# Kernel optimization log

Hardware: AMD Instinct MI355X
Metric: run time of the kernel (lower is better)

The kernel has to match this reference:

```python
import jax, jax.numpy as jnp
import numpy as np

NORM_EPS = 1e-5
HEAD_DIM = 32
SR_RATIO = 2
N_RATIO = SR_RATIO ** 2  # avg-pool kernel/stride over sequence


def setup_inputs() -> dict:
    key = jax.random.key(0)
    ks = jax.random.split(key, 12)
    B, N, C = 4, 3136, 384
    s = 0.02
    inp = {
        "x": jax.random.normal(ks[0], (B, N, C), dtype=jnp.float32),
        "Wq": jax.random.normal(ks[1], (C, C), dtype=jnp.float32) * s,
        "bq": jnp.zeros((C,), jnp.float32),
        "Wk": jax.random.normal(ks[2], (C, C), dtype=jnp.float32) * s,
        "bk": jnp.zeros((C,), jnp.float32),
        "Wv": jax.random.normal(ks[3], (C, C), dtype=jnp.float32) * s,
        "bv": jnp.zeros((C,), jnp.float32),
        "Wp": jax.random.normal(ks[4], (C, C), dtype=jnp.float32) * s,
        "bp": jnp.zeros((C,), jnp.float32),
        "bn_gamma": jnp.ones((C,), jnp.float32),
        "bn_beta": jnp.zeros((C,), jnp.float32),
        "bn_mean": jax.random.normal(ks[5], (C,), dtype=jnp.float32) * 0.1,
        "bn_var": jax.random.uniform(ks[6], (C,), dtype=jnp.float32, minval=0.5, maxval=1.5),
    }
    return inp


def reference(x, Wq, bq, Wk, bk, Wv, bv, Wp, bp, bn_gamma, bn_beta, bn_mean, bn_var):
    B, N, C = x.shape
    H = C // HEAD_DIM
    d = HEAD_DIM
    scale = d ** -0.5

    # q projection -> [B, H, N, d]
    q = (x @ Wq.T + bq).reshape(B, N, H, d)

    # sequence reduction: AvgPool1d(kernel=stride=N_RATIO) over tokens
    Nk = N // N_RATIO
    x_ = x.reshape(B, Nk, N_RATIO, C).mean(axis=2)  # [B, Nk, C]
    # BatchNorm1d over channel dim (inference / running-stats form)
    x_ = (x_ - bn_mean) * jax.lax.rsqrt(bn_var + NORM_EPS) * bn_gamma + bn_beta

    k = (x_ @ Wk.T + bk).reshape(B, Nk, H, d)
    v = (x_ @ Wv.T + bv).reshape(B, Nk, H, d)

    attn = jnp.einsum("bnhd,bmhd->bhnm", q, k) * scale  # [B, H, N, Nk]
    attn = jax.nn.softmax(attn, axis=-1)
    out = jnp.einsum("bhnm,bmhd->bnhd", attn, v).reshape(B, N, C)
    return out @ Wp.T + bp
```

## Files before the change

### kernel.cpp

```cpp
#include <hip/hip_runtime.h>


typedef __bf16 bf16x8 __attribute__((ext_vector_type(8)));
typedef unsigned short u16x8 __attribute__((ext_vector_type(8)));
typedef float f32x4 __attribute__((ext_vector_type(4)));

#define NTOK 3136
#define NKV 784
#define CCH 384
#define KPAD 832
#define SC2 0.25503472078024693f

#define WAIT_BAR(N) asm volatile("s_waitcnt vmcnt(" #N ")\n\ts_barrier" ::: "memory")

__device__ __forceinline__ unsigned short f2b(float f) {
  union { float f; unsigned u; } v; v.f = f;
  unsigned r = v.u + 0x7fffu + ((v.u >> 16) & 1u);
  return (unsigned short)(r >> 16);
}

__device__ __forceinline__ bf16x8 ldsb8(const unsigned short* p) {
  u16x8 v = *(const u16x8*)p;
  return __builtin_bit_cast(bf16x8, v);
}

__device__ __forceinline__ void gload16(const void* g, void* lds) {
  auto* g1 = reinterpret_cast<const __attribute__((address_space(1))) unsigned int*>(
      reinterpret_cast<uintptr_t>(g));
  auto* l3 = reinterpret_cast<__attribute__((address_space(3))) unsigned int*>(
      reinterpret_cast<uintptr_t>(lds));
  __builtin_amdgcn_global_load_lds(g1, l3, 16, 0, 0);
}

__global__ __launch_bounds__(256) void prep_kernel(
    const float* __restrict__ x, const float* __restrict__ gam,
    const float* __restrict__ bet, const float* __restrict__ mea,
    const float* __restrict__ var,
    const float* __restrict__ Wq, const float* __restrict__ Wk,
    const float* __restrict__ Wv, const float* __restrict__ Wp,
    unsigned short* __restrict__ xb, unsigned short* __restrict__ xpb,
    unsigned short* __restrict__ wq, unsigned short* __restrict__ wk,
    unsigned short* __restrict__ wv, unsigned short* __restrict__ wp,
    unsigned short* __restrict__ vt) {
  int bid = blockIdx.x;
  if (bid < 1176) {
    int i = bid * 256 + threadIdx.x;
    int c4 = i % 96;
    int row = i / 96;
    int b = row / NKV, nk = row - b * NKV;
    const float4* x4 = (const float4*)x;
    size_t base = ((size_t)(b * NTOK + nk * 4)) * 96 + c4;
    float sx = 0.f, sy = 0.f, sz = 0.f, sw = 0.f;
#pragma unroll
    for (int r = 0; r < 4; ++r) {
      float4 v = x4[base + (size_t)r * 96];
      ushort4 cv; cv.x = f2b(v.x); cv.y = f2b(v.y); cv.z = f2b(v.z); cv.w = f2b(v.w);
      ((ushort4*)xb)[base + (size_t)r * 96] = cv;
      sx += v.x; sy += v.y; sz += v.z; sw += v.w;
    }
    float4 g4 = ((const float4*)gam)[c4];
    float4 b4 = ((const float4*)bet)[c4];
    float4 m4 = ((const float4*)mea)[c4];
    float4 v4 = ((const float4*)var)[c4];
    ushort4 r4;
    r4.x = f2b((sx * 0.25f - m4.x) * rsqrtf(v4.x + 1e-5f) * g4.x + b4.x);
    r4.y = f2b((sy * 0.25f - m4.y) * rsqrtf(v4.y + 1e-5f) * g4.y + b4.y);
    r4.z = f2b((sz * 0.25f - m4.z) * rsqrtf(v4.z + 1e-5f) * g4.z + b4.z);
    r4.w = f2b((sw * 0.25f - m4.w) * rsqrtf(v4.w + 1e-5f) * g4.w + b4.w);
    ((ushort4*)xpb)[i] = r4;
  } else if (bid < 1320) {
    int i = (bid - 1176) * 256 + threadIdx.x;
    float4 va = ((const float4*)Wq)[i];
    float4 vb = ((const float4*)Wk)[i];
    float4 vc = ((const float4*)Wv)[i];
    float4 vd = ((const float4*)Wp)[i];
    ushort4 ra; ra.x = f2b(va.x); ra.y = f2b(va.y); ra.z = f2b(va.z); ra.w = f2b(va.w);
    ushort4 rb; rb.x = f2b(vb.x); rb.y = f2b(vb.y); rb.z = f2b(vb.z); rb.w = f2b(vb.w);
    ushort4 rc; rc.x = f2b(vc.x); rc.y = f2b(vc.y); rc.z = f2b(vc.z); rc.w = f2b(vc.w);
    ushort4 rd; rd.x = f2b(vd.x); rd.y = f2b(vd.y); rd.z = f2b(vd.z); rd.w = f2b(vd.w);
    ((ushort4*)wq)[i] = ra; ((ushort4*)wk)[i] = rb;
    ((ushort4*)wv)[i] = rc; ((ushort4*)wp)[i] = rd;
  } else {
    int i = (bid - 1320) * 256 + threadIdx.x;
    int row = i >> 4, quad = i & 15;
    ushort4 z; z.x = 0; z.y = 0; z.z = 0; z.w = 0;
    *(ushort4*)&vt[(size_t)row * KPAD + 768 + quad * 4] = z;
  }
}

__device__ __forceinline__ void gemm_body(
    const unsigned short* __restrict__ A, const unsigned short* __restrict__ Bt,
    const float* __restrict__ bias, void* __restrict__ out,
    int row0, int col0, int epi, float oscale,
    unsigned short (*sA)[2048], unsigned short (*sB)[4096]) {
  const int t = threadIdx.x, w = t >> 6, l = t & 63;
  const int wr = w >> 1, wc = w & 1;

  f32x4 acc[2][4];
#pragma unroll
  for (int m = 0; m < 2; ++m)
#pragma unroll
    for (int n = 0; n < 4; ++n) acc[m][n] = (f32x4){0.f, 0.f, 0.f, 0.f};

  const unsigned short* Abase = A + (size_t)(row0 + l) * CCH + w * 8;
  const unsigned short* B0base = Bt + (size_t)(col0 + l) * CCH + w * 8;
  const unsigned short* B1base = Bt + (size_t)(col0 + 64 + l) * CCH + w * 8;

  auto STAGE = [&](int kk, int bsel) {
    gload16(Abase + kk * 32, (char*)sA[bsel] + w * 1024);
    gload16(B0base + kk * 32, (char*)sB[bsel] + w * 2048);
    gload16(B1base + kk * 32, (char*)sB[bsel] + w * 2048 + 1024);
  };

  STAGE(0, 0);
  STAGE(1, 1);
  WAIT_BAR(3);

#pragma unroll
  for (int kk = 0; kk < 12; ++kk) {
    const int cur = kk % 3;
    const int stg = (kk + 2) % 3;
    if (kk + 2 < 12) STAGE(kk + 2, stg);
    bf16x8 af[2], bfv[4];
#pragma unroll
    for (int m = 0; m < 2; ++m)
      af[m] = ldsb8(&sA[cur][(l >> 4) * 512 + (wr * 32 + m * 16 + (l & 15)) * 8]);
#pragma unroll
    for (int n = 0; n < 4; ++n)
      bfv[n] = ldsb8(&sB[cur][(l >> 4) * 1024 + (wc * 64 + n * 16 + (l & 15)) * 8]);
#pragma unroll
    for (int m = 0; m < 2; ++m)
#pragma unroll
      for (int n = 0; n < 4; ++n)
        acc[m][n] = __builtin_amdgcn_mfma_f32_16x16x32_bf16(af[m], bfv[n], acc[m][n], 0, 0, 0);
    if (kk + 1 < 12) {
      if (kk + 2 < 12) WAIT_BAR(3); else WAIT_BAR(0);
    }
  }

#pragma unroll
  for (int m = 0; m < 2; ++m) {
#pragma unroll
    for (int r = 0; r < 4; ++r) {
      int row = row0 + wr * 32 + m * 16 + (l >> 4) * 4 + r;
#pragma unroll
      for (int n = 0; n < 4; ++n) {
        int col = col0 + wc * 64 + n * 16 + (l & 15);
        float v = (acc[m][n][r] + bias[col]) * oscale;
        if (epi == 0) {
          ((unsigned short*)out)[(size_t)row * CCH + col] =
              __builtin_bit_cast(unsigned short, (__bf16)v);
        } else if (epi == 2) {
          ((float*)out)[(size_t)row * CCH + col] = v;
        } else {
          int b_ = row / NKV, j = row - b_ * NKV;
          int h_ = col >> 5, d = col & 31;
          int loc = j & 63;
          int kap = (j & ~63) + ((loc & 16) << 1) + ((loc & 12) << 1) +
                    ((loc & 32) >> 3) + (loc & 3);
          ((unsigned short*)out)[((size_t)((b_ * 12 + h_) * 32 + d)) * KPAD + kap] =
              __builtin_bit_cast(unsigned short, (__bf16)v);
        }
      }
    }
  }
}

__global__ __launch_bounds__(256) void qkv_kernel(
    const unsigned short* __restrict__ xb, const unsigned short* __restrict__ xpb,
    const unsigned short* __restrict__ wq, const unsigned short* __restrict__ wk,
    const unsigned short* __restrict__ wv,
    const float* __restrict__ bq, const float* __restrict__ bk,
    const float* __restrict__ bv,
    unsigned short* __restrict__ q_b, unsigned short* __restrict__ k_b,
    unsigned short* __restrict__ vt_b) {
  __shared__ unsigned short sA[3][2048];
  __shared__ unsigned short sB[3][4096];
  int bx = blockIdx.x;
  const unsigned short *Ap, *Wp_;
  const float* bp_;
  void* op;
  int epi, row0;
  float osc;
  if (bx < 196)      { Ap = xb;  Wp_ = wq; bp_ = bq; op = q_b;  epi = 0; row0 = bx * 64;         osc = SC2; }
  else if (bx < 245) { Ap = xpb; Wp_ = wk; bp_ = bk; op = k_b;  epi = 0; row0 = (bx - 196) * 64; osc = 1.f; }
  else               { Ap = xpb; Wp_ = wv; bp_ = bv; op = vt_b; epi = 1; row0 = (bx - 245) * 64; osc = 1.f; }
  gemm_body(Ap, Wp_, bp_, op, row0, blockIdx.y * 128, epi, osc, sA, sB);
}

__global__ __launch_bounds__(256) void outproj_kernel(
    const unsigned short* __restrict__ ob, const unsigned short* __restrict__ wp,
    const float* __restrict__ bp_, float* __restrict__ out) {
  __shared__ unsigned short sA[3][2048];
  __shared__ unsigned short sB[3][4096];
  gemm_body(ob, wp, bp_, (void*)out, blockIdx.x * 64, blockIdx.y * 128, 2, 1.f, sA, sB);
}

__global__ __launch_bounds__(256) void attn_kernel(
    const unsigned short* __restrict__ qb, const unsigned short* __restrict__ kb,
    const unsigned short* __restrict__ vtb, unsigned short* __restrict__ ob) {
  __shared__ unsigned short sQ[2048];
  __shared__ unsigned short sK[3][2048];
  __shared__ unsigned short sV[3][2048];

  const int bx = blockIdx.x;
  const int qt = bx % 49;
  const int h = (bx / 49) % 12;
  const int b = bx / 588;
  const int t = threadIdx.x, w = t >> 6, l = t & 63;
  const int q0 = qt * 64;
  const int hi = l >> 4, c = l & 15;

  const unsigned short* vbase = vtb + ((size_t)((b * 12 + h) * 32 + (l & 31))) * KPAD
                                + (2 * w + (l >> 5)) * 8;

  auto stageK = [&](int ttile, int bsel) {
    int j = ttile * 64 + l; if (j > NKV - 1) j = NKV - 1;
    gload16(kb + ((size_t)(b * NKV + j)) * CCH + h * 32 + w * 8,
            (char*)sK[bsel] + w * 1024);
  };
  auto stageV = [&](int ttile, int bsel) {
    gload16(vbase + ttile * 64, (char*)sV[bsel] + w * 1024);
  };

  gload16(qb + ((size_t)(b * NTOK + q0 + l)) * CCH + h * 32 + w * 8,
          (char*)sQ + w * 1024);
  stageK(0, 0); stageV(0, 0);
  stageK(1, 1); stageV(1, 1);
  WAIT_BAR(2);

  const bf16x8 aq = ldsb8(&sQ[hi * 512 + (w * 16 + c) * 8]);
  bf16x8 ones;
#pragma unroll
  for (int i = 0; i < 8; ++i) ones[i] = (__bf16)1.0f;
  const f32x4 fz = (f32x4){0.f, 0.f, 0.f, 0.f};

  f32x4 acc0 = fz, acc1 = fz, accl = fz;

#pragma unroll
  for (int tt = 0; tt < 13; ++tt) {
    const int cur = tt % 3;
    const int stg = (tt + 2) % 3;
    if (tt + 2 < 13) { stageK(tt + 2, stg); stageV(tt + 2, stg); }

    f32x4 s[4];
#pragma unroll
    for (int n = 0; n < 4; ++n) {
      bf16x8 kf = ldsb8(&sK[cur][hi * 512 + (n * 16 + c) * 8]);
      s[n] = __builtin_amdgcn_mfma_f32_16x16x32_bf16(kf, aq, fz, 0, 0, 0);
    }

    float p[4][4];
#pragma unroll
    for (int n = 0; n < 4; ++n)
#pragma unroll
      for (int r = 0; r < 4; ++r) {
        float e;
        asm("v_exp_f32 %0, %1" : "=v"(e) : "v"(s[n][r]));
        p[n][r] = e;
      }
    if (tt == 12) {
#pragma unroll
      for (int n = 1; n < 4; ++n)
#pragma unroll
        for (int r = 0; r < 4; ++r) p[n][r] = 0.f;
    }

    bf16x8 pa0, pa1;
#pragma unroll
    for (int rr = 0; rr < 4; ++rr) {
      pa0[rr] = (__bf16)p[0][rr];
      pa0[4 + rr] = (__bf16)p[2][rr];
      pa1[rr] = (__bf16)p[1][rr];
      pa1[4 + rr] = (__bf16)p[3][rr];
    }

#pragma unroll
    for (int kkk = 0; kkk < 2; ++kkk) {
      bf16x8 pa = kkk ? pa1 : pa0;
      bf16x8 v0 = ldsb8(&sV[cur][(kkk * 4 + hi) * 256 + c * 8]);
      bf16x8 v1 = ldsb8(&sV[cur][(kkk * 4 + hi) * 256 + (16 + c) * 8]);
      acc0 = __builtin_amdgcn_mfma_f32_16x16x32_bf16(pa, v0, acc0, 0, 0, 0);
      acc1 = __builtin_amdgcn_mfma_f32_16x16x32_bf16(pa, v1, acc1, 0, 0, 0);
      accl = __builtin_amdgcn_mfma_f32_16x16x32_bf16(pa, ones, accl, 0, 0, 0);
    }

    if (tt + 1 < 13) {
      if (tt + 2 < 13) WAIT_BAR(2); else WAIT_BAR(0);
    }
  }

#pragma unroll
  for (int r = 0; r < 4; ++r) {
    int row = q0 + w * 16 + hi * 4 + r;
    float inv = 1.f / accl[r];
    size_t base = ((size_t)(b * NTOK + row)) * CCH + h * 32;
    ob[base + c] = __builtin_bit_cast(unsigned short, (__bf16)(acc0[r] * inv));
    ob[base + 16 + c] = __builtin_bit_cast(unsigned short, (__bf16)(acc1[r] * inv));
  }
}


extern "C" void kernel_launch(void* const* d_in, const int* in_sizes, int n_in,
                              void* d_out, int out_size, void* d_ws, size_t ws_size,
                              hipStream_t stream) {
  const float* x   = (const float*)d_in[0];
  const float* Wq  = (const float*)d_in[1];
  const float* bq  = (const float*)d_in[2];
  const float* Wk  = (const float*)d_in[3];
  const float* bk  = (const float*)d_in[4];
  const float* Wv  = (const float*)d_in[5];
  const float* bv  = (const float*)d_in[6];
  const float* Wp  = (const float*)d_in[7];
  const float* bp  = (const float*)d_in[8];
  const float* gam = (const float*)d_in[9];
  const float* bet = (const float*)d_in[10];
  const float* mea = (const float*)d_in[11];
  const float* var = (const float*)d_in[12];

  unsigned short* wq_b = (unsigned short*)d_ws;
  unsigned short* wk_b = wq_b + 147456;
  unsigned short* wv_b = wk_b + 147456;
  unsigned short* wp_b = wv_b + 147456;
  unsigned short* xb   = wp_b + 147456;
  unsigned short* x_b  = xb + 12544 * 384;
  unsigned short* q_b  = x_b + 3136 * 384;
  unsigned short* k_b  = q_b + 12544 * 384;
  unsigned short* vt_b = k_b + 3136 * 384;
  unsigned short* o_b  = vt_b + 1536 * KPAD;

  prep_kernel<<<1416, 256, 0, stream>>>(x, gam, bet, mea, var, Wq, Wk, Wv, Wp,
                                        xb, x_b, wq_b, wk_b, wv_b, wp_b, vt_b);
  qkv_kernel<<<dim3(294, 3), 256, 0, stream>>>(xb, x_b, wq_b, wk_b, wv_b,
                                               bq, bk, bv, q_b, k_b, vt_b);
  attn_kernel<<<2352, 256, 0, stream>>>(q_b, k_b, vt_b, o_b);
  outproj_kernel<<<dim3(196, 3), 256, 0, stream>>>(o_b, wp_b, bp, (float*)d_out);
}
```

Before: 95.00 us.

## Double row tiles to 128 in Q/out-proj GEMMs and attention query tiles

Templates the GEMM body on the row-tile size, so the Q projection and the output projection use 128-row tiles while the K/V projections keep 64 rows. The attention kernel now handles 128 query rows per block with two Q fragments, so each staged K/V tile is reused for twice as many queries, with clamped loads and a guarded store for the partial last tile. The intent is to cut redundant global and LDS loads of weights and K/V and to lower block count overhead. In exchange the grids are smaller, which may hurt load balance and occupancy, and register and LDS use per block goes up.

```diff
diff --git a/kernel.cpp b/kernel.cpp
--- a/kernel.cpp
+++ b/kernel.cpp
@@ -88,64 +88,79 @@
   }
 }
 
+template <int MR>
 __device__ __forceinline__ void gemm_body(
     const unsigned short* __restrict__ A, const unsigned short* __restrict__ Bt,
     const float* __restrict__ bias, void* __restrict__ out,
     int row0, int col0, int epi, float oscale,
-    unsigned short (*sA)[2048], unsigned short (*sB)[4096]) {
+    unsigned short* sA, unsigned short* sB) {
+  constexpr int ABUF = MR * 32;
+  constexpr int MH = MR / 2;
+  constexpr int NM = MR / 32;
   const int t = threadIdx.x, w = t >> 6, l = t & 63;
   const int wr = w >> 1, wc = w & 1;
-
-  f32x4 acc[2][4];
-#pragma unroll
-  for (int m = 0; m < 2; ++m)
+  const int hi = l >> 4, c = l & 15;
+
+  f32x4 acc[NM][4];
+#pragma unroll
+  for (int m = 0; m < NM; ++m)
 #pragma unroll
     for (int n = 0; n < 4; ++n) acc[m][n] = (f32x4){0.f, 0.f, 0.f, 0.f};
 
   const unsigned short* Abase = A + (size_t)(row0 + l) * CCH + w * 8;
+  const unsigned short* Abase2 = A + (size_t)(row0 + 64 + l) * CCH + w * 8;
   const unsigned short* B0base = Bt + (size_t)(col0 + l) * CCH + w * 8;
   const unsigned short* B1base = Bt + (size_t)(col0 + 64 + l) * CCH + w * 8;
 
   auto STAGE = [&](int kk, int bsel) {
-    gload16(Abase + kk * 32, (char*)sA[bsel] + w * 1024);
-    gload16(B0base + kk * 32, (char*)sB[bsel] + w * 2048);
-    gload16(B1base + kk * 32, (char*)sB[bsel] + w * 2048 + 1024);
+    if constexpr (MR == 128) {
+      gload16(Abase + kk * 32, (char*)(sA + bsel * ABUF) + w * 2048);
+      gload16(Abase2 + kk * 32, (char*)(sA + bsel * ABUF) + w * 2048 + 1024);
+    } else {
+      gload16(Abase + kk * 32, (char*)(sA + bsel * ABUF) + w * 1024);
+    }
+    gload16(B0base + kk * 32, (char*)(sB + bsel * 4096) + w * 2048);
+    gload16(B1base + kk * 32, (char*)(sB + bsel * 4096) + w * 2048 + 1024);
   };
 
   STAGE(0, 0);
   STAGE(1, 1);
-  WAIT_BAR(3);
+  if constexpr (MR == 128) WAIT_BAR(4); else WAIT_BAR(3);
 
 #pragma unroll
   for (int kk = 0; kk < 12; ++kk) {
     const int cur = kk % 3;
     const int stg = (kk + 2) % 3;
     if (kk + 2 < 12) STAGE(kk + 2, stg);
-    bf16x8 af[2], bfv[4];
-#pragma unroll
-    for (int m = 0; m < 2; ++m)
-      af[m] = ldsb8(&sA[cur][(l >> 4) * 512 + (wr * 32 + m * 16 + (l & 15)) * 8]);
+    bf16x8 af[NM], bfv[4];
+#pragma unroll
+    for (int m = 0; m < NM; ++m)
+      af[m] = ldsb8(sA + cur * ABUF + hi * (MR * 8) + (wr * MH + m * 16 + c) * 8);
 #pragma unroll
     for (int n = 0; n < 4; ++n)
-      bfv[n] = ldsb8(&sB[cur][(l >> 4) * 1024 + (wc * 64 + n * 16 + (l & 15)) * 8]);
-#pragma unroll
-    for (int m = 0; m < 2; ++m)
+      bfv[n] = ldsb8(sB + cur * 4096 + hi * 1024 + (wc * 64 + n * 16 + c) * 8);
+#pragma unroll
+    for (int m = 0; m < NM; ++m)
 #pragma unroll
       for (int n = 0; n < 4; ++n)
         acc[m][n] = __builtin_amdgcn_mfma_f32_16x16x32_bf16(af[m], bfv[n], acc[m][n], 0, 0, 0);
     if (kk + 1 < 12) {
-      if (kk + 2 < 12) WAIT_BAR(3); else WAIT_BAR(0);
-    }
-  }
-
-#pragma unroll
-  for (int m = 0; m < 2; ++m) {
+      if (kk + 2 < 12) {
+        if constexpr (MR == 128) WAIT_BAR(4); else WAIT_BAR(3);
+      } else {
+        WAIT_BAR(0);
+      }
+    }
+  }
+
+#pragma unroll
+  for (int m = 0; m < NM; ++m) {
 #pragma unroll
     for (int r = 0; r < 4; ++r) {
-      int row = row0 + wr * 32 + m * 16 + (l >> 4) * 4 + r;
+      int row = row0 + wr * MH + m * 16 + hi * 4 + r;
 #pragma unroll
       for (int n = 0; n < 4; ++n) {
-        int col = col0 + wc * 64 + n * 16 + (l & 15);
+        int col = col0 + wc * 64 + n * 16 + c;
         float v = (acc[m][n][r] + bias[col]) * oscale;
         if (epi == 0) {
           ((unsigned short*)out)[(size_t)row * CCH + col] =
@@ -174,41 +189,40 @@
     const float* __restrict__ bv,
     unsigned short* __restrict__ q_b, unsigned short* __restrict__ k_b,
     unsigned short* __restrict__ vt_b) {
-  __shared__ unsigned short sA[3][2048];
-  __shared__ unsigned short sB[3][4096];
-  int bx = blockIdx.x;
-  const unsigned short *Ap, *Wp_;
-  const float* bp_;
-  void* op;
-  int epi, row0;
-  float osc;
-  if (bx < 196)      { Ap = xb;  Wp_ = wq; bp_ = bq; op = q_b;  epi = 0; row0 = bx * 64;         osc = SC2; }
-  else if (bx < 245) { Ap = xpb; Wp_ = wk; bp_ = bk; op = k_b;  epi = 0; row0 = (bx - 196) * 64; osc = 1.f; }
-  else               { Ap = xpb; Wp_ = wv; bp_ = bv; op = vt_b; epi = 1; row0 = (bx - 245) * 64; osc = 1.f; }
-  gemm_body(Ap, Wp_, bp_, op, row0, blockIdx.y * 128, epi, osc, sA, sB);
+  __shared__ unsigned short sA[3 * 4096];
+  __shared__ unsigned short sB[3 * 4096];
+  int bx = blockIdx.x, cy = blockIdx.y * 128;
+  if (bx < 98) {
+    gemm_body<128>(xb, wq, bq, (void*)q_b, bx * 128, cy, 0, SC2, sA, sB);
+  } else if (bx < 147) {
+    gemm_body<64>(xpb, wk, bk, (void*)k_b, (bx - 98) * 64, cy, 0, 1.f, sA, sB);
+  } else {
+    gemm_body<64>(xpb, wv, bv, (void*)vt_b, (bx - 147) * 64, cy, 1, 1.f, sA, sB);
+  }
 }
 
 __global__ __launch_bounds__(256) void outproj_kernel(
     const unsigned short* __restrict__ ob, const unsigned short* __restrict__ wp,
     const float* __restrict__ bp_, float* __restrict__ out) {
-  __shared__ unsigned short sA[3][2048];
-  __shared__ unsigned short sB[3][4096];
-  gemm_body(ob, wp, bp_, (void*)out, blockIdx.x * 64, blockIdx.y * 128, 2, 1.f, sA, sB);
+  __shared__ unsigned short sA[3 * 4096];
+  __shared__ unsigned short sB[3 * 4096];
+  gemm_body<128>(ob, wp, bp_, (void*)out, blockIdx.x * 128, blockIdx.y * 128, 2, 1.f,
+                 sA, sB);
 }
 
 __global__ __launch_bounds__(256) void attn_kernel(
     const unsigned short* __restrict__ qb, const unsigned short* __restrict__ kb,
     const unsigned short* __restrict__ vtb, unsigned short* __restrict__ ob) {
-  __shared__ unsigned short sQ[2048];
+  __shared__ unsigned short sQ[4096];
   __shared__ unsigned short sK[3][2048];
   __shared__ unsigned short sV[3][2048];
 
   const int bx = blockIdx.x;
-  const int qt = bx % 49;
-  const int h = (bx / 49) % 12;
-  const int b = bx / 588;
+  const int qt = bx % 25;
+  const int h = (bx / 25) % 12;
+  const int b = bx / 300;
   const int t = threadIdx.x, w = t >> 6, l = t & 63;
-  const int q0 = qt * 64;
+  const int q0 = qt * 128;
   const int hi = l >> 4, c = l & 15;
 
   const unsigned short* vbase = vtb + ((size_t)((b * 12 + h) * 32 + (l & 31))) * KPAD
@@ -223,19 +237,27 @@
     gload16(vbase + ttile * 64, (char*)sV[bsel] + w * 1024);
   };
 
-  gload16(qb + ((size_t)(b * NTOK + q0 + l)) * CCH + h * 32 + w * 8,
-          (char*)sQ + w * 1024);
+  {
+    int r0 = q0 + l;            if (r0 > NTOK - 1) r0 = NTOK - 1;
+    int r1 = q0 + 64 + l;       if (r1 > NTOK - 1) r1 = NTOK - 1;
+    gload16(qb + ((size_t)(b * NTOK + r0)) * CCH + h * 32 + w * 8,
+            (char*)sQ + w * 1024);
+    gload16(qb + ((size_t)(b * NTOK + r1)) * CCH + h * 32 + w * 8,
+            (char*)sQ + 4096 + w * 1024);
+  }
   stageK(0, 0); stageV(0, 0);
   stageK(1, 1); stageV(1, 1);
   WAIT_BAR(2);
 
-  const bf16x8 aq = ldsb8(&sQ[hi * 512 + (w * 16 + c) * 8]);
+  const bf16x8 aq0 = ldsb8(&sQ[hi * 512 + (w * 16 + c) * 8]);
+  const bf16x8 aq1 = ldsb8(&sQ[2048 + hi * 512 + (w * 16 + c) * 8]);
   bf16x8 ones;
 #pragma unroll
   for (int i = 0; i < 8; ++i) ones[i] = (__bf16)1.0f;
   const f32x4 fz = (f32x4){0.f, 0.f, 0.f, 0.f};
 
-  f32x4 acc0 = fz, acc1 = fz, accl = fz;
+  f32x4 a00 = fz, a01 = fz, al0 = fz;
+  f32x4 a10 = fz, a11 = fz, al1 = fz;
 
 #pragma unroll
   for (int tt = 0; tt < 13; ++tt) {
@@ -243,46 +265,70 @@
     const int stg = (tt + 2) % 3;
     if (tt + 2 < 13) { stageK(tt + 2, stg); stageV(tt + 2, stg); }
 
-    f32x4 s[4];
+    f32x4 s0[4], s1[4];
 #pragma unroll
     for (int n = 0; n < 4; ++n) {
       bf16x8 kf = ldsb8(&sK[cur][hi * 512 + (n * 16 + c) * 8]);
-      s[n] = __builtin_amdgcn_mfma_f32_16x16x32_bf16(kf, aq, fz, 0, 0, 0);
-    }
-
-    float p[4][4];
-#pragma unroll
-    for (int n = 0; n < 4; ++n)
-#pragma unroll
-      for (int r = 0; r < 4; ++r) {
-        float e;
-        asm("v_exp_f32 %0, %1" : "=v"(e) : "v"(s[n][r]));
-        p[n][r] = e;
+      s0[n] = __builtin_amdgcn_mfma_f32_16x16x32_bf16(kf, aq0, fz, 0, 0, 0);
+      s1[n] = __builtin_amdgcn_mfma_f32_16x16x32_bf16(kf, aq1, fz, 0, 0, 0);
+    }
+
+    bf16x8 pa00, pa01, pa10, pa11;
+    {
+      float p[4][4];
+#pragma unroll
+      for (int n = 0; n < 4; ++n)
+#pragma unroll
+        for (int r = 0; r < 4; ++r) {
+          float e;
+          asm("v_exp_f32 %0, %1" : "=v"(e) : "v"(s0[n][r]));
+          p[n][r] = e;
+        }
+      if (tt == 12)
+#pragma unroll
+        for (int n = 1; n < 4; ++n)
+#pragma unroll
+          for (int r = 0; r < 4; ++r) p[n][r] = 0.f;
+#pragma unroll
+      for (int rr = 0; rr < 4; ++rr) {
+        pa00[rr] = (__bf16)p[0][rr]; pa00[4 + rr] = (__bf16)p[2][rr];
+        pa01[rr] = (__bf16)p[1][rr]; pa01[4 + rr] = (__bf16)p[3][rr];
       }
-    if (tt == 12) {
-#pragma unroll
-      for (int n = 1; n < 4; ++n)
-#pragma unroll
-        for (int r = 0; r < 4; ++r) p[n][r] = 0.f;
-    }
-
-    bf16x8 pa0, pa1;
-#pragma unroll
-    for (int rr = 0; rr < 4; ++rr) {
-      pa0[rr] = (__bf16)p[0][rr];
-      pa0[4 + rr] = (__bf16)p[2][rr];
-      pa1[rr] = (__bf16)p[1][rr];
-      pa1[4 + rr] = (__bf16)p[3][rr];
+    }
+    {
+      float p[4][4];
+#pragma unroll
+      for (int n = 0; n < 4; ++n)
+#pragma unroll
+        for (int r = 0; r < 4; ++r) {
+          float e;
+          asm("v_exp_f32 %0, %1" : "=v"(e) : "v"(s1[n][r]));
+          p[n][r] = e;
+        }
+      if (tt == 12)
+#pragma unroll
+        for (int n = 1; n < 4; ++n)
+#pragma unroll
+          for (int r = 0; r < 4; ++r) p[n][r] = 0.f;
+#pragma unroll
+      for (int rr = 0; rr < 4; ++rr) {
+        pa10[rr] = (__bf16)p[0][rr]; pa10[4 + rr] = (__bf16)p[2][rr];
+        pa11[rr] = (__bf16)p[1][rr]; pa11[4 + rr] = (__bf16)p[3][rr];
+      }
     }
 
 #pragma unroll
     for (int kkk = 0; kkk < 2; ++kkk) {
-      bf16x8 pa = kkk ? pa1 : pa0;
+      bf16x8 pg0 = kkk ? pa01 : pa00;
+      bf16x8 pg1 = kkk ? pa11 : pa10;
       bf16x8 v0 = ldsb8(&sV[cur][(kkk * 4 + hi) * 256 + c * 8]);
       bf16x8 v1 = ldsb8(&sV[cur][(kkk * 4 + hi) * 256 + (16 + c) * 8]);
-      acc0 = __builtin_amdgcn_mfma_f32_16x16x32_bf16(pa, v0, acc0, 0, 0, 0);
-      acc1 = __builtin_amdgcn_mfma_f32_16x16x32_bf16(pa, v1, acc1, 0, 0, 0);
-      accl = __builtin_amdgcn_mfma_f32_16x16x32_bf16(pa, ones, accl, 0, 0, 0);
+      a00 = __builtin_amdgcn_mfma_f32_16x16x32_bf16(pg0, v0, a00, 0, 0, 0);
+      a10 = __builtin_amdgcn_mfma_f32_16x16x32_bf16(pg1, v0, a10, 0, 0, 0);
+      a01 = __builtin_amdgcn_mfma_f32_16x16x32_bf16(pg0, v1, a01, 0, 0, 0);
+      a11 = __builtin_amdgcn_mfma_f32_16x16x32_bf16(pg1, v1, a11, 0, 0, 0);
+      al0 = __builtin_amdgcn_mfma_f32_16x16x32_bf16(pg0, ones, al0, 0, 0, 0);
+      al1 = __builtin_amdgcn_mfma_f32_16x16x32_bf16(pg1, ones, al1, 0, 0, 0);
     }
 
     if (tt + 1 < 13) {
@@ -293,10 +339,20 @@
 #pragma unroll
   for (int r = 0; r < 4; ++r) {
     int row = q0 + w * 16 + hi * 4 + r;
-    float inv = 1.f / accl[r];
+    float inv = 1.f / al0[r];
     size_t base = ((size_t)(b * NTOK + row)) * CCH + h * 32;
-    ob[base + c] = __builtin_bit_cast(unsigned short, (__bf16)(acc0[r] * inv));
-    ob[base + 16 + c] = __builtin_bit_cast(unsigned short, (__bf16)(acc1[r] * inv));
+    ob[base + c] = __builtin_bit_cast(unsigned short, (__bf16)(a00[r] * inv));
+    ob[base + 16 + c] = __builtin_bit_cast(unsigned short, (__bf16)(a01[r] * inv));
+  }
+#pragma unroll
+  for (int r = 0; r < 4; ++r) {
+    int row = q0 + 64 + w * 16 + hi * 4 + r;
+    if (row < NTOK) {
+      float inv = 1.f / al1[r];
+      size_t base = ((size_t)(b * NTOK + row)) * CCH + h * 32;
+      ob[base + c] = __builtin_bit_cast(unsigned short, (__bf16)(a10[r] * inv));
+      ob[base + 16 + c] = __builtin_bit_cast(unsigned short, (__bf16)(a11[r] * inv));
+    }
   }
 }
 
@@ -331,8 +387,8 @@
 
   prep_kernel<<<1416, 256, 0, stream>>>(x, gam, bet, mea, var, Wq, Wk, Wv, Wp,
                                         xb, x_b, wq_b, wk_b, wv_b, wp_b, vt_b);
-  qkv_kernel<<<dim3(294, 3), 256, 0, stream>>>(xb, x_b, wq_b, wk_b, wv_b,
+  qkv_kernel<<<dim3(196, 3), 256, 0, stream>>>(xb, x_b, wq_b, wk_b, wv_b,
                                                bq, bk, bv, q_b, k_b, vt_b);
-  attn_kernel<<<2352, 256, 0, stream>>>(q_b, k_b, vt_b, o_b);
-  outproj_kernel<<<dim3(196, 3), 256, 0, stream>>>(o_b, wp_b, bp, (float*)d_out);
-}
+  attn_kernel<<<1200, 256, 0, stream>>>(q_b, k_b, vt_b, o_b);
+  outproj_kernel<<<dim3(98, 3), 256, 0, stream>>>(o_b, wp_b, bp, (float*)d_out);
+}
```

Result: faster. 79.21 us (-16.6%).
